# Performance work log

Measured on AMD Instinct MI355X. Metric: run time of the kernel, lower is better.

## Reference

```python
import jax, jax.numpy as jnp
import numpy as np

NUM_HEADS = 32
NUM_KV_HEADS = 8
HEAD_DIM = 128
N_REP = NUM_HEADS // NUM_KV_HEADS
ROPE_BASE = 10000.0
NEG_INF = -3.4e38  # large negative for causal mask (matches fp32 min magnitude behavior)


def setup_inputs() -> dict:
    key = jax.random.key(0)
    ks = jax.random.split(key, 5)
    B, S, D = 1, 2048, 4096
    KV = NUM_KV_HEADS * HEAD_DIM  # 1024
    scale = 0.02
    return {
        "hidden_states": jax.random.normal(ks[0], (B, S, D), dtype=jnp.float32),
        "Wq": jax.random.normal(ks[1], (D, D), dtype=jnp.float32) * scale,
        "Wk": jax.random.normal(ks[2], (D, KV), dtype=jnp.float32) * scale,
        "Wv": jax.random.normal(ks[3], (D, KV), dtype=jnp.float32) * scale,
        "Wo": jax.random.normal(ks[4], (D, D), dtype=jnp.float32) * scale,
    }


def _rotate_half(x):
    x1, x2 = jnp.split(x, 2, axis=-1)
    return jnp.concatenate((-x2, x1), axis=-1)


def _rope_cos_sin(B, S, dtype):
    # Qwen/Llama-style rotary embedding, base 10000, position_ids = arange(S)
    inv_freq = 1.0 / (ROPE_BASE ** (jnp.arange(0, HEAD_DIM, 2, dtype=jnp.float32) / HEAD_DIM))
    pos = jnp.arange(S, dtype=jnp.float32)[None, :]            # [1, S] (broadcast over batch)
    freqs = pos[..., None] * inv_freq[None, None, :]           # [1, S, D/2]
    emb = jnp.concatenate((freqs, freqs), axis=-1)             # [1, S, D]
    return jnp.cos(emb).astype(dtype), jnp.sin(emb).astype(dtype)


def reference(hidden_states, Wq, Wk, Wv, Wo):
    B, S, D = hidden_states.shape
    dtype = hidden_states.dtype

    q = (hidden_states @ Wq).reshape(B, S, NUM_HEADS, HEAD_DIM).transpose(0, 2, 1, 3)      # [B,H,S,d]
    k = (hidden_states @ Wk).reshape(B, S, NUM_KV_HEADS, HEAD_DIM).transpose(0, 2, 1, 3)   # [B,Hkv,S,d]
    v = (hidden_states @ Wv).reshape(B, S, NUM_KV_HEADS, HEAD_DIM).transpose(0, 2, 1, 3)

    cos, sin = _rope_cos_sin(B, S, dtype)
    cos = cos[:, None, :, :]  # unsqueeze head dim
    sin = sin[:, None, :, :]
    q = q * cos + _rotate_half(q) * sin
    k = k * cos + _rotate_half(k) * sin

    # repeat_kv: [B,Hkv,S,d] -> [B,H,S,d]
    k = jnp.repeat(k, N_REP, axis=1)
    v = jnp.repeat(v, N_REP, axis=1)

    attn = jnp.einsum("bhqd,bhkd->bhqk", q, k) / jnp.sqrt(jnp.asarray(HEAD_DIM, dtype))
    causal = jnp.where(jnp.arange(S)[:, None] >= jnp.arange(S)[None, :], 0.0, NEG_INF).astype(dtype)
    attn = attn + causal[None, None, :, :]
    attn = jax.nn.softmax(attn.astype(jnp.float32), axis=-1).astype(dtype)

    out = jnp.einsum("bhqk,bhkd->bhqd", attn, v)           # [B,H,S,d]
    out = out.transpose(0, 2, 1, 3).reshape(B, S, NUM_HEADS * HEAD_DIM)
    return out @ Wo
```

## Files before the change

### kernel.cpp

```cpp
#include <hip/hip_runtime.h>
#include <stdint.h>

typedef float f32x4 __attribute__((ext_vector_type(4)));
typedef __bf16 bf16x8 __attribute__((ext_vector_type(8)));
typedef unsigned short u16;
typedef unsigned short u16x8 __attribute__((ext_vector_type(8)));

__device__ __forceinline__ u16 f2b(float f) {
    union { float f; unsigned u; } v; v.f = f;
    return (u16)((v.u + 0x7fffu + ((v.u >> 16) & 1u)) >> 16);
}
__device__ __forceinline__ float b2f(u16 b) {
    union { unsigned u; float f; } v; v.u = ((unsigned)b) << 16;
    return v.f;
}

__device__ __forceinline__ void gload16(const u16* g, u16* s) {
    __builtin_amdgcn_global_load_lds((const __attribute__((address_space(1))) void*)g,
                                     (__attribute__((address_space(3))) void*)s, 16, 0, 0);
}

__global__ __launch_bounds__(256) void k_cast(const float* __restrict__ src, u16* __restrict__ dst, int n) {
    int i = (blockIdx.x * 256 + threadIdx.x) * 8;
    if (i >= n) return;
    const float4* s = (const float4*)(src + i);
    float4 a = s[0], b = s[1];
    u16x8 o;
    o[0] = f2b(a.x); o[1] = f2b(a.y); o[2] = f2b(a.z); o[3] = f2b(a.w);
    o[4] = f2b(b.x); o[5] = f2b(b.y); o[6] = f2b(b.z); o[7] = f2b(b.w);
    *(u16x8*)(dst + i) = o;
}

__global__ __launch_bounds__(256) void k_transpose(const float* __restrict__ src, u16* __restrict__ dst,
                                                   int R, int C) {
    __shared__ float tile[64][65];
    int c0 = blockIdx.x * 64, r0 = blockIdx.y * 64;
    int tx = threadIdx.x & 63, ty = threadIdx.x >> 6;
    #pragma unroll
    for (int r = ty; r < 64; r += 4)
        tile[r][tx] = src[(size_t)(r0 + r) * C + (c0 + tx)];
    __syncthreads();
    #pragma unroll
    for (int r = ty; r < 64; r += 4)
        dst[(size_t)(c0 + r) * R + (r0 + tx)] = f2b(tile[tx][r]);
}

__global__ __launch_bounds__(256) void k_vt(const u16* __restrict__ V, u16* __restrict__ VT) {
    __shared__ u16 tile[64][66];
    int kh = blockIdx.z;
    int s0 = blockIdx.y * 64;
    int d0 = blockIdx.x * 64;
    int tx = threadIdx.x & 63, ty = threadIdx.x >> 6;
    #pragma unroll
    for (int r = ty; r < 64; r += 4)
        tile[r][tx] = V[(size_t)(s0 + r) * 1024 + kh * 128 + d0 + tx];
    __syncthreads();
    #pragma unroll
    for (int r = ty; r < 64; r += 4)
        VT[(size_t)kh * 262144 + (size_t)(d0 + r) * 2048 + s0 + tx] = tile[tx][r];
}

#define STAGE_A(h) do { \
    _Pragma("unroll") for (int i_ = 0; i_ < MFR / 4; ++i_) \
        gload16(gA + (size_t)((h) * (MFR * 16) + i_ * 8) * K + kn, &Ah[nb][h][w * (MFR * 2) + i_ * 8][0]); \
} while (0)
#define STAGE_B(h) do { \
    gload16(gB + (size_t)((h) * 128) * K + kn,     &Bh[nb][h][w * 16][0]);     \
    gload16(gB + (size_t)((h) * 128 + 8) * K + kn, &Bh[nb][h][w * 16 + 8][0]); } while (0)
#define RD_AF(MH, AF) do { \
    _Pragma("unroll") for (int mm = 0; mm < MFR / 2; ++mm) \
    _Pragma("unroll") for (int x = 0; x < 2; ++x) \
        AF[mm][x] = *(const bf16x8*)&Ah[c][wm][((MH) * (MFR / 2) + mm) * 16 + lr][(x * 32 + lk) ^ swz]; } while (0)
#define RD_BF(NH, BF) do { \
    _Pragma("unroll") for (int nn = 0; nn < 2; ++nn) \
    _Pragma("unroll") for (int x = 0; x < 2; ++x) \
        BF[nn][x] = *(const bf16x8*)&Bh[c][wn >> 1][(wn & 1) * 64 + ((NH) * 2 + nn) * 16 + lr][(x * 32 + lk) ^ swz]; } while (0)
#define MMAQ(MH, NH, AF, BF) do { \
    _Pragma("unroll") for (int x = 0; x < 2; ++x) \
    _Pragma("unroll") for (int mm = 0; mm < MFR / 2; ++mm) \
    _Pragma("unroll") for (int nn = 0; nn < 2; ++nn) \
        acc[(MH) * (MFR / 2) + mm][(NH) * 2 + nn] = __builtin_amdgcn_mfma_f32_16x16x32_bf16( \
            AF[mm][x], BF[nn][x], acc[(MH) * (MFR / 2) + mm][(NH) * 2 + nn], 0, 0, 0); } while (0)

template <int MFR, typename OutT>
__device__ __forceinline__ void gemm256_core(const u16* __restrict__ A, const u16* __restrict__ Bt,
                                             OutT* __restrict__ C, int K, int ldc, int m0, int n0) {
    __shared__ u16 Ah[2][2][MFR * 16][64];
    __shared__ u16 Bh[2][2][128][64];
    constexpr int LPT = 2 * (MFR / 4) + 4;
    int tid = threadIdx.x;
    int l = tid & 63, w = tid >> 6;
    int wm = w >> 2, wn = w & 3;
    int lr = l & 15, lg = l >> 4, lk = lg * 8;
    int swz = (lr & 7) << 3;
    int srow8 = l >> 3;
    int scol = ((l & 7) ^ srow8) * 8;
    const u16* gA = A  + (size_t)(m0 + w * (MFR * 2) + srow8) * K + scol;
    const u16* gB = Bt + (size_t)(n0 + w * 16 + srow8) * K + scol;
    f32x4 acc[MFR][4] = {};
    int NT = K >> 6;

    {
        int kn = 0, nb = 0;
        STAGE_B(0); STAGE_B(1); STAGE_A(0); STAGE_A(1);
    }

    #pragma unroll 2
    for (int t = 0; t < NT; ++t) {
        int c = t & 1, nb = c ^ 1;
        int kn = (t + 1) << 6;
        bool last = (t == NT - 1);
        bf16x8 af0[MFR / 2][2], af1[MFR / 2][2], bf0[2][2], bf1[2][2];
        if (!last) {
            STAGE_B(0); STAGE_B(1); STAGE_A(0); STAGE_A(1);
            asm volatile("s_waitcnt vmcnt(%0)" :: "n"(LPT) : "memory");
        } else {
            asm volatile("s_waitcnt vmcnt(0)" ::: "memory");
        }
        __builtin_amdgcn_s_barrier();
        RD_AF(0, af0); RD_BF(0, bf0);
        __builtin_amdgcn_s_setprio(1);
        MMAQ(0, 0, af0, bf0);
        __builtin_amdgcn_s_setprio(0);
        RD_BF(1, bf1);
        __builtin_amdgcn_s_setprio(1);
        MMAQ(0, 1, af0, bf1);
        __builtin_amdgcn_s_setprio(0);
        RD_AF(1, af1);
        __builtin_amdgcn_s_setprio(1);
        MMAQ(1, 1, af1, bf1);
        MMAQ(1, 0, af1, bf0);
        __builtin_amdgcn_s_setprio(0);
        __builtin_amdgcn_s_barrier();
    }

    #pragma unroll
    for (int m = 0; m < MFR; ++m)
        #pragma unroll
        for (int n = 0; n < 4; ++n)
            #pragma unroll
            for (int e = 0; e < 4; ++e) {
                int row = m0 + wm * (MFR * 16) + m * 16 + lg * 4 + e;
                int col = n0 + wn * 64 + n * 16 + lr;
                if constexpr (sizeof(OutT) == 4)
                    C[(size_t)row * ldc + col] = acc[m][n][e];
                else
                    C[(size_t)row * ldc + col] = f2b(acc[m][n][e]);
            }
}

__global__ __launch_bounds__(512, 2) void k_gemm_qkv(const u16* __restrict__ hsb,
        const u16* __restrict__ WqT, const u16* __restrict__ WkT, const u16* __restrict__ WvT,
        u16* __restrict__ Qb, u16* __restrict__ Kb, u16* __restrict__ Vb) {
    int bid = blockIdx.x;
    int ord = (bid & 7) * 24 + (bid >> 3);
    int mt = ord / 24, nt = ord % 24;
    const u16* Bt; u16* Cd; int ldc, n0;
    if (nt < 16)      { Bt = WqT; Cd = Qb; ldc = 4096; n0 = nt * 256; }
    else if (nt < 20) { Bt = WkT; Cd = Kb; ldc = 1024; n0 = (nt - 16) * 256; }
    else              { Bt = WvT; Cd = Vb; ldc = 1024; n0 = (nt - 20) * 256; }
    gemm256_core<8, u16>(hsb, Bt, Cd, 4096, ldc, mt * 256, n0);
}

__global__ __launch_bounds__(512, 2) void k_gemm_out(const u16* __restrict__ Ob, const u16* __restrict__ WoT,
                                                     float* __restrict__ out) {
    int bid = blockIdx.x;
    int ord = (bid & 7) * 32 + (bid >> 3);
    int mt = ord >> 4, nt = ord & 15;
    gemm256_core<4, float>(Ob, WoT, out, 4096, 4096, mt * 128, nt * 256);
}

__global__ __launch_bounds__(256) void k_rope(u16* __restrict__ Qb, u16* __restrict__ Kb) {
    int t = blockIdx.x * 256 + threadIdx.x;
    int i = t & 63;
    int rest = t >> 6;
    int head = rest % 40;
    int s = rest / 40;
    if (s >= 2048) return;
    u16* base = (head < 32) ? (Qb + (size_t)s * 4096 + head * 128)
                            : (Kb + (size_t)s * 1024 + (head - 32) * 128);
    float inv = exp2f((float)i * (-13.287712379549449f / 64.0f));
    float fr = (float)s * inv;
    float sn, cs;
    sincosf(fr, &sn, &cs);
    float x1 = b2f(base[i]), x2 = b2f(base[i + 64]);
    base[i]      = f2b(x1 * cs - x2 * sn);
    base[i + 64] = f2b(x2 * cs + x1 * sn);
}

__global__ __launch_bounds__(256, 2) void k_attn(const u16* __restrict__ Q, const u16* __restrict__ K,
                                                 const u16* __restrict__ VT, u16* __restrict__ O) {
    __shared__ u16 Kl[2][64][128];
    __shared__ u16 VTl[128][64];
    __shared__ u16 Pl[4][32][68];
    int bid = blockIdx.x;
    int kh = bid & 7;
    int x = bid >> 3;
    int j = x >> 2;
    int h = kh * 4 + (x & 3);
    int qb = (j < 8) ? j : 23 - j;
    int q0 = qb * 128;
    int t = threadIdx.x, l = t & 63, w = t >> 6;
    int lr = l & 15, lg = l >> 4;
    const float cexp = 0.12751742f;
    const u16* Kh = K + kh * 128;
    const u16* VTh = VT + (size_t)kh * 262144;

#define ATT_STAGE_K(B, KV0) do { \
    _Pragma("unroll") for (int i_ = 0; i_ < 4; ++i_) { \
        int r0_ = w * 16 + i_ * 4; \
        int row_ = r0_ + (l >> 4); \
        gload16(Kh + (size_t)((KV0) + row_) * 1024 + ((l & 15) ^ (row_ & 7)) * 8, \
                &Kl[B][r0_][0]); \
    } } while (0)
#define ATT_STAGE_V(KV0) do { \
    _Pragma("unroll") for (int i_ = 0; i_ < 4; ++i_) { \
        int r0_ = w * 32 + i_ * 8; \
        int row_ = r0_ + (l >> 3); \
        gload16(VTh + (size_t)row_ * 2048 + (KV0) + ((l & 7) ^ (row_ & 7)) * 8, \
                &VTl[r0_][0]); \
    } } while (0)

    bf16x8 qf[2][4];
    #pragma unroll
    for (int rb = 0; rb < 2; ++rb) {
        size_t qoff = (size_t)(q0 + w * 32 + rb * 16 + lr) * 4096 + h * 128 + lg * 8;
        #pragma unroll
        for (int d = 0; d < 4; ++d)
            qf[rb][d] = *(const bf16x8*)(Q + qoff + d * 32);
    }
    bf16x8 ones;
    #pragma unroll
    for (int i = 0; i < 8; ++i) ones[i] = (__bf16)1.0f;

    f32x4 oacc[2][8] = {};
    f32x4 osum[2] = {};
    float mrow[2][4];
    #pragma unroll
    for (int rb = 0; rb < 2; ++rb)
        #pragma unroll
        for (int e = 0; e < 4; ++e) mrow[rb][e] = -3.0e38f;

    int ntiles = 2 * qb + 2;
    int rowmax = q0 + w * 32 + 31;

    ATT_STAGE_K(0, 0);

    for (int kt = 0; kt < ntiles; ++kt) {
        int ck = kt & 1;
        int kv0 = kt * 64;
        bool compute = (kv0 <= rowmax);
        bool more = (kt + 1 < ntiles);
        asm volatile("s_waitcnt vmcnt(0)" ::: "memory");
        __builtin_amdgcn_s_barrier();
        ATT_STAGE_V(kv0);
        if (more) ATT_STAGE_K(ck ^ 1, kv0 + 64);
        __builtin_amdgcn_sched_barrier(0);

        f32x4 sacc[2][4] = {};
        if (compute) {
            #pragma unroll
            for (int d = 0; d < 4; ++d) {
                bf16x8 kf[4];
                #pragma unroll
                for (int cb = 0; cb < 4; ++cb)
                    kf[cb] = *(const bf16x8*)&Kl[ck][cb * 16 + lr][((d * 4 + lg) ^ (lr & 7)) * 8];
                #pragma unroll
                for (int cb = 0; cb < 4; ++cb) {
                    sacc[0][cb] = __builtin_amdgcn_mfma_f32_16x16x32_bf16(qf[0][d], kf[cb], sacc[0][cb], 0, 0, 0);
                    sacc[1][cb] = __builtin_amdgcn_mfma_f32_16x16x32_bf16(qf[1][d], kf[cb], sacc[1][cb], 0, 0, 0);
                }
            }
            if (kt >= 2 * qb) {
                #pragma unroll
                for (int rb = 0; rb < 2; ++rb)
                    #pragma unroll
                    for (int cb = 0; cb < 4; ++cb)
                        #pragma unroll
                        for (int e = 0; e < 4; ++e) {
                            int row = q0 + w * 32 + rb * 16 + lg * 4 + e;
                            int col = kv0 + cb * 16 + lr;
                            if (col > row) sacc[rb][cb][e] = -3.0e38f;
                        }
            }
            float vmax[2][4];
            bool need = false;
            #pragma unroll
            for (int rb = 0; rb < 2; ++rb)
                #pragma unroll
                for (int e = 0; e < 4; ++e) {
                    float v = fmaxf(fmaxf(sacc[rb][0][e], sacc[rb][1][e]), fmaxf(sacc[rb][2][e], sacc[rb][3][e]));
                    v = fmaxf(v, __shfl_xor(v, 1));
                    v = fmaxf(v, __shfl_xor(v, 2));
                    v = fmaxf(v, __shfl_xor(v, 4));
                    v = fmaxf(v, __shfl_xor(v, 8));
                    vmax[rb][e] = v;
                    need = need || (v > mrow[rb][e] + 62.0f);
                }
            if (__any(need)) {
                #pragma unroll
                for (int rb = 0; rb < 2; ++rb)
                    #pragma unroll
                    for (int e = 0; e < 4; ++e) {
                        float mnew = fmaxf(mrow[rb][e], vmax[rb][e]);
                        float alpha = exp2f((mrow[rb][e] - mnew) * cexp);
                        mrow[rb][e] = mnew;
                        osum[rb][e] *= alpha;
                        #pragma unroll
                        for (int db = 0; db < 8; ++db) oacc[rb][db][e] *= alpha;
                    }
            }
            #pragma unroll
            for (int rb = 0; rb < 2; ++rb)
                #pragma unroll
                for (int cb = 0; cb < 4; ++cb)
                    #pragma unroll
                    for (int e = 0; e < 4; ++e)
                        Pl[w][rb * 16 + lg * 4 + e][cb * 16 + lr] =
                            f2b(exp2f((sacc[rb][cb][e] - mrow[rb][e]) * cexp));
        }
        if (more) asm volatile("s_waitcnt vmcnt(4)" ::: "memory");
        else      asm volatile("s_waitcnt vmcnt(0)" ::: "memory");
        __builtin_amdgcn_s_barrier();
        if (compute) {
            asm volatile("s_waitcnt lgkmcnt(0)" ::: "memory");
            __builtin_amdgcn_sched_barrier(0);
            __builtin_amdgcn_s_setprio(1);
            #pragma unroll
            for (int ks = 0; ks < 2; ++ks) {
                bf16x8 pf0 = *(const bf16x8*)&Pl[w][lr][ks * 32 + lg * 8];
                bf16x8 pf1 = *(const bf16x8*)&Pl[w][16 + lr][ks * 32 + lg * 8];
                osum[0] = __builtin_amdgcn_mfma_f32_16x16x32_bf16(pf0, ones, osum[0], 0, 0, 0);
                osum[1] = __builtin_amdgcn_mfma_f32_16x16x32_bf16(pf1, ones, osum[1], 0, 0, 0);
                #pragma unroll
                for (int db = 0; db < 8; ++db) {
                    bf16x8 vf = *(const bf16x8*)&VTl[db * 16 + lr][((ks * 4 + lg) ^ (lr & 7)) * 8];
                    oacc[0][db] = __builtin_amdgcn_mfma_f32_16x16x32_bf16(pf0, vf, oacc[0][db], 0, 0, 0);
                    oacc[1][db] = __builtin_amdgcn_mfma_f32_16x16x32_bf16(pf1, vf, oacc[1][db], 0, 0, 0);
                }
            }
            __builtin_amdgcn_s_setprio(0);
        }
    }
    #pragma unroll
    for (int rb = 0; rb < 2; ++rb)
        #pragma unroll
        for (int db = 0; db < 8; ++db)
            #pragma unroll
            for (int e = 0; e < 4; ++e) {
                int row = q0 + w * 32 + rb * 16 + lg * 4 + e;
                O[(size_t)row * 4096 + h * 128 + db * 16 + lr] = f2b(oacc[rb][db][e] / osum[rb][e]);
            }
#undef ATT_STAGE_K
#undef ATT_STAGE_V
}

extern "C" void kernel_launch(void* const* d_in, const int* in_sizes, int n_in,
                              void* d_out, int out_size, void* d_ws, size_t ws_size,
                              hipStream_t stream) {
    const float* hs = (const float*)d_in[0];
    const float* Wq = (const float*)d_in[1];
    const float* Wk = (const float*)d_in[2];
    const float* Wv = (const float*)d_in[3];
    const float* Wo = (const float*)d_in[4];
    float* out = (float*)d_out;
    char* ws = (char*)d_ws;
    u16* hsb = (u16*)(ws);
    u16* WqT = (u16*)(ws + 16777216);
    u16* WkT = (u16*)(ws + 50331648);
    u16* WvT = (u16*)(ws + 58720256);
    u16* Qb  = (u16*)(ws + 67108864);
    u16* Kb  = (u16*)(ws + 83886080);
    u16* Vb  = (u16*)(ws + 88080384);

    k_cast<<<4096, 256, 0, stream>>>(hs, hsb, 2048 * 4096);
    k_transpose<<<dim3(64, 64), 256, 0, stream>>>(Wq, WqT, 4096, 4096);
    k_transpose<<<dim3(16, 64), 256, 0, stream>>>(Wk, WkT, 4096, 1024);
    k_transpose<<<dim3(16, 64), 256, 0, stream>>>(Wv, WvT, 4096, 1024);
    k_gemm_qkv<<<192, 512, 0, stream>>>(hsb, WqT, WkT, WvT, Qb, Kb, Vb);
    k_rope<<<20480, 256, 0, stream>>>(Qb, Kb);
    u16* VTb = WkT;
    k_vt<<<dim3(2, 32, 8), 256, 0, stream>>>(Vb, VTb);
    u16* Ob = hsb;
    k_attn<<<512, 256, 0, stream>>>(Qb, Kb, VTb, Ob);
    u16* WoT = WqT;
    k_transpose<<<dim3(64, 64), 256, 0, stream>>>(Wo, WoT, 4096, 4096);
    k_gemm_out<<<256, 512, 0, stream>>>(Ob, WoT, out);
}
```

Before: 386.2 us.

## Interleave global-to-LDS staging with MFMA phases in GEMM mainloop

Restructures the double-buffered GEMM mainloop into an explicitly unrolled even/odd pair. Each of the four MFMA quadrants is now preceded by issuing one slice of the next tile's global-to-LDS loads, instead of all loads at the top of the iteration. Barriers and lgkmcnt waits fence each phase so loads, LDS reads and MFMAs overlap more evenly across the warps. The cost is many more barriers per iteration. It also assumes the tile count along K is even, with a finer vmcnt accounting that must stay correct.

```diff
diff --git a/kernel.cpp b/kernel.cpp
--- a/kernel.cpp
+++ b/kernel.cpp
@@ -81,13 +81,20 @@
     _Pragma("unroll") for (int nn = 0; nn < 2; ++nn) \
         acc[(MH) * (MFR / 2) + mm][(NH) * 2 + nn] = __builtin_amdgcn_mfma_f32_16x16x32_bf16( \
             AF[mm][x], BF[nn][x], acc[(MH) * (MFR / 2) + mm][(NH) * 2 + nn], 0, 0, 0); } while (0)
+#define PH_SYNC do { __builtin_amdgcn_s_barrier(); \
+                     asm volatile("s_waitcnt lgkmcnt(0)" ::: "memory"); \
+                     __builtin_amdgcn_sched_barrier(0); } while (0)
+#define PH_MMA(MH, NH, AF, BF) do { __builtin_amdgcn_s_setprio(1); \
+                                    MMAQ(MH, NH, AF, BF); \
+                                    __builtin_amdgcn_s_setprio(0); \
+                                    __builtin_amdgcn_s_barrier(); } while (0)
 
 template <int MFR, typename OutT>
 __device__ __forceinline__ void gemm256_core(const u16* __restrict__ A, const u16* __restrict__ Bt,
                                              OutT* __restrict__ C, int K, int ldc, int m0, int n0) {
     __shared__ u16 Ah[2][2][MFR * 16][64];
     __shared__ u16 Bh[2][2][128][64];
-    constexpr int LPT = 2 * (MFR / 4) + 4;
+    constexpr int VMC = (MFR == 8) ? 2 : 1;
     int tid = threadIdx.x;
     int l = tid & 63, w = tid >> 6;
     int wm = w >> 2, wn = w & 3;
@@ -100,38 +107,49 @@
     f32x4 acc[MFR][4] = {};
     int NT = K >> 6;
 
-    {
-        int kn = 0, nb = 0;
-        STAGE_B(0); STAGE_B(1); STAGE_A(0); STAGE_A(1);
-    }
-
-    #pragma unroll 2
-    for (int t = 0; t < NT; ++t) {
-        int c = t & 1, nb = c ^ 1;
-        int kn = (t + 1) << 6;
-        bool last = (t == NT - 1);
+    { int kn = 0,  nb = 0; STAGE_A(0); STAGE_B(0); STAGE_B(1); STAGE_A(1); }
+    { int kn = 64, nb = 1; STAGE_A(0); }
+    asm volatile("s_waitcnt vmcnt(%0)" :: "n"(VMC) : "memory");
+    __builtin_amdgcn_s_barrier();
+
+    for (int it = 0; it < NT / 2; ++it) {
+        int tE = 2 * it, tO = 2 * it + 1;
+        bool more = (it < NT / 2 - 1);
         bf16x8 af0[MFR / 2][2], af1[MFR / 2][2], bf0[2][2], bf1[2][2];
-        if (!last) {
-            STAGE_B(0); STAGE_B(1); STAGE_A(0); STAGE_A(1);
-            asm volatile("s_waitcnt vmcnt(%0)" :: "n"(LPT) : "memory");
-        } else {
-            asm volatile("s_waitcnt vmcnt(0)" ::: "memory");
+        {
+            int c = 0;
+            RD_AF(0, af0); RD_BF(0, bf0);
+            { int kn = tO << 6, nb = 1; STAGE_B(0); }
+            PH_SYNC;  PH_MMA(0, 0, af0, bf0);
+            RD_BF(1, bf1);
+            { int kn = tO << 6, nb = 1; STAGE_B(1); }
+            PH_SYNC;  PH_MMA(0, 1, af0, bf1);
+            RD_AF(1, af1);
+            { int kn = tO << 6, nb = 1; STAGE_A(1); }
+            PH_SYNC;  PH_MMA(1, 1, af1, bf1);
+            if (more) { int kn = (tE + 2) << 6, nb = 0; STAGE_A(0); }
+            if (more) asm volatile("s_waitcnt vmcnt(%0)" :: "n"(VMC) : "memory");
+            else      asm volatile("s_waitcnt vmcnt(0)" ::: "memory");
+            __builtin_amdgcn_s_barrier();
+            PH_MMA(1, 0, af1, bf0);
         }
-        __builtin_amdgcn_s_barrier();
-        RD_AF(0, af0); RD_BF(0, bf0);
-        __builtin_amdgcn_s_setprio(1);
-        MMAQ(0, 0, af0, bf0);
-        __builtin_amdgcn_s_setprio(0);
-        RD_BF(1, bf1);
-        __builtin_amdgcn_s_setprio(1);
-        MMAQ(0, 1, af0, bf1);
-        __builtin_amdgcn_s_setprio(0);
-        RD_AF(1, af1);
-        __builtin_amdgcn_s_setprio(1);
-        MMAQ(1, 1, af1, bf1);
-        MMAQ(1, 0, af1, bf0);
-        __builtin_amdgcn_s_setprio(0);
-        __builtin_amdgcn_s_barrier();
+        {
+            int c = 1;
+            RD_AF(0, af0); RD_BF(0, bf0);
+            if (more) { int kn = (tE + 2) << 6, nb = 0; STAGE_B(0); }
+            PH_SYNC;  PH_MMA(0, 0, af0, bf0);
+            RD_BF(1, bf1);
+            if (more) { int kn = (tE + 2) << 6, nb = 0; STAGE_B(1); }
+            PH_SYNC;  PH_MMA(0, 1, af0, bf1);
+            RD_AF(1, af1);
+            if (more) { int kn = (tE + 2) << 6, nb = 0; STAGE_A(1); }
+            PH_SYNC;  PH_MMA(1, 1, af1, bf1);
+            if (more) { int kn = (tO + 2) << 6, nb = 1; STAGE_A(0); }
+            if (more) asm volatile("s_waitcnt vmcnt(%0)" :: "n"(VMC) : "memory");
+            else      asm volatile("s_waitcnt vmcnt(0)" ::: "memory");
+            __builtin_amdgcn_s_barrier();
+            PH_MMA(1, 0, af1, bf0);
+        }
     }
 
     #pragma unroll
```

Result: slower. 416.8 us (+7.9%).

## Fuse QKV weights into one matrix and retile GEMM to 256x192

Applied to the files above, without the earlier changes.

Concatenates the transposed Wq/Wk/Wv into a single 6144-column weight and writes Q, K and V into one interleaved buffer with a 6144 row stride. The QKV GEMM core is generalised to a configurable N fragment count and uses 256x192 tiles, giving 256 blocks instead of 192 so the grid fills the GPU more evenly. Rope, V-transpose and attention index into the fused buffer, and the Wo transpose is moved earlier into a different workspace slot. Costs are the wider strides for K/Q reads in attention and a different B-staging pattern.

```diff
diff --git a/kernel.cpp b/kernel.cpp
--- a/kernel.cpp
+++ b/kernel.cpp
@@ -45,7 +45,7 @@
         dst[(size_t)(c0 + r) * R + (r0 + tx)] = f2b(tile[tx][r]);
 }
 
-__global__ __launch_bounds__(256) void k_vt(const u16* __restrict__ V, u16* __restrict__ VT) {
+__global__ __launch_bounds__(256) void k_vt(const u16* __restrict__ QKV, u16* __restrict__ VT) {
     __shared__ u16 tile[64][66];
     int kh = blockIdx.z;
     int s0 = blockIdx.y * 64;
@@ -53,7 +53,7 @@
     int tx = threadIdx.x & 63, ty = threadIdx.x >> 6;
     #pragma unroll
     for (int r = ty; r < 64; r += 4)
-        tile[r][tx] = V[(size_t)(s0 + r) * 1024 + kh * 128 + d0 + tx];
+        tile[r][tx] = QKV[(size_t)(s0 + r) * 6144 + 5120 + kh * 128 + d0 + tx];
     __syncthreads();
     #pragma unroll
     for (int r = ty; r < 64; r += 4)
@@ -64,30 +64,30 @@
     _Pragma("unroll") for (int i_ = 0; i_ < MFR / 4; ++i_) \
         gload16(gA + (size_t)((h) * (MFR * 16) + i_ * 8) * K + kn, &Ah[nb][h][w * (MFR * 2) + i_ * 8][0]); \
 } while (0)
-#define STAGE_B(h) do { \
-    gload16(gB + (size_t)((h) * 128) * K + kn,     &Bh[nb][h][w * 16][0]);     \
-    gload16(gB + (size_t)((h) * 128 + 8) * K + kn, &Bh[nb][h][w * 16 + 8][0]); } while (0)
+#define STAGE_B1(h) gload16(gB + (size_t)((h) * 64) * K + kn, &Bh[nb][h][w * 8][0])
+#define STAGE_ALL do { \
+    _Pragma("unroll") for (int h_ = 0; h_ < 2; ++h_) STAGE_A(h_); \
+    _Pragma("unroll") for (int h_ = 0; h_ < NFR; ++h_) STAGE_B1(h_); } while (0)
 #define RD_AF(MH, AF) do { \
     _Pragma("unroll") for (int mm = 0; mm < MFR / 2; ++mm) \
     _Pragma("unroll") for (int x = 0; x < 2; ++x) \
         AF[mm][x] = *(const bf16x8*)&Ah[c][wm][((MH) * (MFR / 2) + mm) * 16 + lr][(x * 32 + lk) ^ swz]; } while (0)
-#define RD_BF(NH, BF) do { \
-    _Pragma("unroll") for (int nn = 0; nn < 2; ++nn) \
+#define RD_BF1(NF) do { \
+    int bc_ = wn * (NFR * 16) + (NF) * 16; \
     _Pragma("unroll") for (int x = 0; x < 2; ++x) \
-        BF[nn][x] = *(const bf16x8*)&Bh[c][wn >> 1][(wn & 1) * 64 + ((NH) * 2 + nn) * 16 + lr][(x * 32 + lk) ^ swz]; } while (0)
-#define MMAQ(MH, NH, AF, BF) do { \
+        bfr[NF][x] = *(const bf16x8*)&Bh[c][bc_ >> 6][(bc_ & 63) + lr][(x * 32 + lk) ^ swz]; } while (0)
+#define MMAH(MH, NF, AF) do { \
     _Pragma("unroll") for (int x = 0; x < 2; ++x) \
     _Pragma("unroll") for (int mm = 0; mm < MFR / 2; ++mm) \
-    _Pragma("unroll") for (int nn = 0; nn < 2; ++nn) \
-        acc[(MH) * (MFR / 2) + mm][(NH) * 2 + nn] = __builtin_amdgcn_mfma_f32_16x16x32_bf16( \
-            AF[mm][x], BF[nn][x], acc[(MH) * (MFR / 2) + mm][(NH) * 2 + nn], 0, 0, 0); } while (0)
-
-template <int MFR, typename OutT>
-__device__ __forceinline__ void gemm256_core(const u16* __restrict__ A, const u16* __restrict__ Bt,
-                                             OutT* __restrict__ C, int K, int ldc, int m0, int n0) {
+        acc[(MH) * (MFR / 2) + mm][NF] = __builtin_amdgcn_mfma_f32_16x16x32_bf16( \
+            AF[mm][x], bfr[NF][x], acc[(MH) * (MFR / 2) + mm][NF], 0, 0, 0); } while (0)
+
+template <int MFR, int NFR, typename OutT>
+__device__ __forceinline__ void gemm_core(const u16* __restrict__ A, const u16* __restrict__ Bt,
+                                          OutT* __restrict__ C, int K, int ldc, int m0, int n0) {
     __shared__ u16 Ah[2][2][MFR * 16][64];
-    __shared__ u16 Bh[2][2][128][64];
-    constexpr int LPT = 2 * (MFR / 4) + 4;
+    __shared__ u16 Bh[2][NFR][64][64];
+    constexpr int LPT = MFR / 2 + NFR;
     int tid = threadIdx.x;
     int l = tid & 63, w = tid >> 6;
     int wm = w >> 2, wn = w & 3;
@@ -96,13 +96,13 @@
     int srow8 = l >> 3;
     int scol = ((l & 7) ^ srow8) * 8;
     const u16* gA = A  + (size_t)(m0 + w * (MFR * 2) + srow8) * K + scol;
-    const u16* gB = Bt + (size_t)(n0 + w * 16 + srow8) * K + scol;
-    f32x4 acc[MFR][4] = {};
+    const u16* gB = Bt + (size_t)(n0 + w * 8 + srow8) * K + scol;
+    f32x4 acc[MFR][NFR] = {};
     int NT = K >> 6;
 
     {
         int kn = 0, nb = 0;
-        STAGE_B(0); STAGE_B(1); STAGE_A(0); STAGE_A(1);
+        STAGE_ALL;
     }
 
     #pragma unroll 2
@@ -110,26 +110,27 @@
         int c = t & 1, nb = c ^ 1;
         int kn = (t + 1) << 6;
         bool last = (t == NT - 1);
-        bf16x8 af0[MFR / 2][2], af1[MFR / 2][2], bf0[2][2], bf1[2][2];
+        bf16x8 af0[MFR / 2][2], af1[MFR / 2][2], bfr[NFR][2];
         if (!last) {
-            STAGE_B(0); STAGE_B(1); STAGE_A(0); STAGE_A(1);
+            STAGE_ALL;
             asm volatile("s_waitcnt vmcnt(%0)" :: "n"(LPT) : "memory");
         } else {
             asm volatile("s_waitcnt vmcnt(0)" ::: "memory");
         }
         __builtin_amdgcn_s_barrier();
-        RD_AF(0, af0); RD_BF(0, bf0);
-        __builtin_amdgcn_s_setprio(1);
-        MMAQ(0, 0, af0, bf0);
-        __builtin_amdgcn_s_setprio(0);
-        RD_BF(1, bf1);
-        __builtin_amdgcn_s_setprio(1);
-        MMAQ(0, 1, af0, bf1);
-        __builtin_amdgcn_s_setprio(0);
+        RD_AF(0, af0);
+        #pragma unroll
+        for (int nf = 0; nf < NFR; ++nf) {
+            RD_BF1(nf);
+            __builtin_amdgcn_s_setprio(1);
+            MMAH(0, nf, af0);
+            __builtin_amdgcn_s_setprio(0);
+        }
         RD_AF(1, af1);
         __builtin_amdgcn_s_setprio(1);
-        MMAQ(1, 1, af1, bf1);
-        MMAQ(1, 0, af1, bf0);
+        #pragma unroll
+        for (int nf = 0; nf < NFR; ++nf)
+            MMAH(1, nf, af1);
         __builtin_amdgcn_s_setprio(0);
         __builtin_amdgcn_s_barrier();
     }
@@ -137,11 +138,11 @@
     #pragma unroll
     for (int m = 0; m < MFR; ++m)
         #pragma unroll
-        for (int n = 0; n < 4; ++n)
+        for (int n = 0; n < NFR; ++n)
             #pragma unroll
             for (int e = 0; e < 4; ++e) {
                 int row = m0 + wm * (MFR * 16) + m * 16 + lg * 4 + e;
-                int col = n0 + wn * 64 + n * 16 + lr;
+                int col = n0 + wn * (NFR * 16) + n * 16 + lr;
                 if constexpr (sizeof(OutT) == 4)
                     C[(size_t)row * ldc + col] = acc[m][n][e];
                 else
@@ -150,16 +151,11 @@
 }
 
 __global__ __launch_bounds__(512, 2) void k_gemm_qkv(const u16* __restrict__ hsb,
-        const u16* __restrict__ WqT, const u16* __restrict__ WkT, const u16* __restrict__ WvT,
-        u16* __restrict__ Qb, u16* __restrict__ Kb, u16* __restrict__ Vb) {
+        const u16* __restrict__ WqkvT, u16* __restrict__ QKVb) {
     int bid = blockIdx.x;
-    int ord = (bid & 7) * 24 + (bid >> 3);
-    int mt = ord / 24, nt = ord % 24;
-    const u16* Bt; u16* Cd; int ldc, n0;
-    if (nt < 16)      { Bt = WqT; Cd = Qb; ldc = 4096; n0 = nt * 256; }
-    else if (nt < 20) { Bt = WkT; Cd = Kb; ldc = 1024; n0 = (nt - 16) * 256; }
-    else              { Bt = WvT; Cd = Vb; ldc = 1024; n0 = (nt - 20) * 256; }
-    gemm256_core<8, u16>(hsb, Bt, Cd, 4096, ldc, mt * 256, n0);
+    int ord = (bid & 7) * 32 + (bid >> 3);
+    int mt = ord >> 5, nt = ord & 31;
+    gemm_core<8, 3, u16>(hsb, WqkvT, QKVb, 4096, 6144, mt * 256, nt * 192);
 }
 
 __global__ __launch_bounds__(512, 2) void k_gemm_out(const u16* __restrict__ Ob, const u16* __restrict__ WoT,
@@ -167,18 +163,18 @@
     int bid = blockIdx.x;
     int ord = (bid & 7) * 32 + (bid >> 3);
     int mt = ord >> 4, nt = ord & 15;
-    gemm256_core<4, float>(Ob, WoT, out, 4096, 4096, mt * 128, nt * 256);
-}
-
-__global__ __launch_bounds__(256) void k_rope(u16* __restrict__ Qb, u16* __restrict__ Kb) {
+    gemm_core<4, 4, float>(Ob, WoT, out, 4096, 4096, mt * 128, nt * 256);
+}
+
+__global__ __launch_bounds__(256) void k_rope(u16* __restrict__ QKV) {
     int t = blockIdx.x * 256 + threadIdx.x;
     int i = t & 63;
     int rest = t >> 6;
     int head = rest % 40;
     int s = rest / 40;
     if (s >= 2048) return;
-    u16* base = (head < 32) ? (Qb + (size_t)s * 4096 + head * 128)
-                            : (Kb + (size_t)s * 1024 + (head - 32) * 128);
+    u16* base = (head < 32) ? (QKV + (size_t)s * 6144 + head * 128)
+                            : (QKV + (size_t)s * 6144 + 4096 + (head - 32) * 128);
     float inv = exp2f((float)i * (-13.287712379549449f / 64.0f));
     float fr = (float)s * inv;
     float sn, cs;
@@ -188,7 +184,7 @@
     base[i + 64] = f2b(x2 * cs + x1 * sn);
 }
 
-__global__ __launch_bounds__(256, 2) void k_attn(const u16* __restrict__ Q, const u16* __restrict__ K,
+__global__ __launch_bounds__(256, 2) void k_attn(const u16* __restrict__ QKV,
                                                  const u16* __restrict__ VT, u16* __restrict__ O) {
     __shared__ u16 Kl[2][64][128];
     __shared__ u16 VTl[128][64];
@@ -203,14 +199,14 @@
     int t = threadIdx.x, l = t & 63, w = t >> 6;
     int lr = l & 15, lg = l >> 4;
     const float cexp = 0.12751742f;
-    const u16* Kh = K + kh * 128;
+    const u16* Kh = QKV + 4096 + kh * 128;
     const u16* VTh = VT + (size_t)kh * 262144;
 
 #define ATT_STAGE_K(B, KV0) do { \
     _Pragma("unroll") for (int i_ = 0; i_ < 4; ++i_) { \
         int r0_ = w * 16 + i_ * 4; \
         int row_ = r0_ + (l >> 4); \
-        gload16(Kh + (size_t)((KV0) + row_) * 1024 + ((l & 15) ^ (row_ & 7)) * 8, \
+        gload16(Kh + (size_t)((KV0) + row_) * 6144 + ((l & 15) ^ (row_ & 7)) * 8, \
                 &Kl[B][r0_][0]); \
     } } while (0)
 #define ATT_STAGE_V(KV0) do { \
@@ -224,10 +220,10 @@
     bf16x8 qf[2][4];
     #pragma unroll
     for (int rb = 0; rb < 2; ++rb) {
-        size_t qoff = (size_t)(q0 + w * 32 + rb * 16 + lr) * 4096 + h * 128 + lg * 8;
+        size_t qoff = (size_t)(q0 + w * 32 + rb * 16 + lr) * 6144 + h * 128 + lg * 8;
         #pragma unroll
         for (int d = 0; d < 4; ++d)
-            qf[rb][d] = *(const bf16x8*)(Q + qoff + d * 32);
+            qf[rb][d] = *(const bf16x8*)(QKV + qoff + d * 32);
     }
     bf16x8 ones;
     #pragma unroll
@@ -365,25 +361,21 @@
     const float* Wo = (const float*)d_in[4];
     float* out = (float*)d_out;
     char* ws = (char*)d_ws;
-    u16* hsb = (u16*)(ws);
-    u16* WqT = (u16*)(ws + 16777216);
-    u16* WkT = (u16*)(ws + 50331648);
-    u16* WvT = (u16*)(ws + 58720256);
-    u16* Qb  = (u16*)(ws + 67108864);
-    u16* Kb  = (u16*)(ws + 83886080);
-    u16* Vb  = (u16*)(ws + 88080384);
+    u16* hsb   = (u16*)(ws);
+    u16* WqkvT = (u16*)(ws + 16777216);
+    u16* QKVb  = (u16*)(ws + 67108864);
 
     k_cast<<<4096, 256, 0, stream>>>(hs, hsb, 2048 * 4096);
-    k_transpose<<<dim3(64, 64), 256, 0, stream>>>(Wq, WqT, 4096, 4096);
-    k_transpose<<<dim3(16, 64), 256, 0, stream>>>(Wk, WkT, 4096, 1024);
-    k_transpose<<<dim3(16, 64), 256, 0, stream>>>(Wv, WvT, 4096, 1024);
-    k_gemm_qkv<<<192, 512, 0, stream>>>(hsb, WqT, WkT, WvT, Qb, Kb, Vb);
-    k_rope<<<20480, 256, 0, stream>>>(Qb, Kb);
-    u16* VTb = WkT;
-    k_vt<<<dim3(2, 32, 8), 256, 0, stream>>>(Vb, VTb);
+    k_transpose<<<dim3(64, 64), 256, 0, stream>>>(Wq, WqkvT, 4096, 4096);
+    k_transpose<<<dim3(16, 64), 256, 0, stream>>>(Wk, WqkvT + (size_t)4096 * 4096, 4096, 1024);
+    k_transpose<<<dim3(16, 64), 256, 0, stream>>>(Wv, WqkvT + (size_t)5120 * 4096, 4096, 1024);
+    k_gemm_qkv<<<256, 512, 0, stream>>>(hsb, WqkvT, QKVb);
+    k_rope<<<20480, 256, 0, stream>>>(QKVb);
+    u16* VTb = WqkvT;
+    k_vt<<<dim3(2, 32, 8), 256, 0, stream>>>(QKVb, VTb);
+    u16* WoT = WqkvT + (size_t)2097152;
+    k_transpose<<<dim3(64, 64), 256, 0, stream>>>(Wo, WoT, 4096, 4096);
     u16* Ob = hsb;
-    k_attn<<<512, 256, 0, stream>>>(Qb, Kb, VTb, Ob);
-    u16* WoT = WqT;
-    k_transpose<<<dim3(64, 64), 256, 0, stream>>>(Wo, WoT, 4096, 4096);
+    k_attn<<<512, 256, 0, stream>>>(QKVb, VTb, Ob);
     k_gemm_out<<<256, 512, 0, stream>>>(Ob, WoT, out);
 }
```

Result: faster. 371.6 us (-3.8%).
